# Kernel optimization log

Measured on AMD Instinct MI355X. Metric: run time of the kernel, lower is better.

The kernel has to match this reference:

```python
import math
import jax, jax.numpy as jnp
import numpy as np

B, T, D, H, L = 8, 2048, 1024, 16, 4
DK = D // H
EPS_LN = 1e-5
EPS_ATTN = 1e-6


def setup_inputs() -> dict:
    key = jax.random.key(0)
    ks = jax.random.split(key, 8)
    w = lambda k, shape: jax.random.normal(k, shape, dtype=jnp.float32) * 0.02
    return {
        'x_in': jax.random.normal(ks[0], (B, T, D), dtype=jnp.float32),
        'Wq': w(ks[1], (L, D, D)), 'bq': jnp.zeros((L, D), jnp.float32),
        'Wk': w(ks[2], (L, D, D)), 'bk': jnp.zeros((L, D), jnp.float32),
        'Wv': w(ks[3], (L, D, D)), 'bv': jnp.zeros((L, D), jnp.float32),
        'Wo': w(ks[4], (L, D, D)), 'bo': jnp.zeros((L, D), jnp.float32),
        'W1': w(ks[5], (L, D, 4 * D)), 'b1': jnp.zeros((L, 4 * D), jnp.float32),
        'W2': w(ks[6], (L, 4 * D, D)), 'b2': jnp.zeros((L, D), jnp.float32),
        'ln1_s': jnp.ones((L, D), jnp.float32), 'ln1_b': jnp.zeros((L, D), jnp.float32),
        'ln2_s': jnp.ones((L, D), jnp.float32), 'ln2_b': jnp.zeros((L, D), jnp.float32),
        'lnf_s': jnp.ones((D,), jnp.float32), 'lnf_b': jnp.zeros((D,), jnp.float32),
    }


def _layernorm(x, scale, bias):
    mu = jnp.mean(x, axis=-1, keepdims=True)
    var = jnp.mean(jnp.square(x - mu), axis=-1, keepdims=True)
    return (x - mu) * jax.lax.rsqrt(var + EPS_LN) * scale + bias


def _sinusoidal_pos_emb(t, d):
    # fairseq/MulT-style: sin half then cos half, positions start at 1 (padding_idx+1)
    half = d // 2
    freq = jnp.exp(jnp.arange(half, dtype=jnp.float32) * (-math.log(10000.0) / (half - 1)))
    pos = (jnp.arange(t, dtype=jnp.float32) + 1.0)[:, None] * freq[None, :]  # (T, half)
    return jnp.concatenate([jnp.sin(pos), jnp.cos(pos)], axis=-1)  # (T, D)


def _linear_attention(q, k, v):
    # q,k,v: (B, T, H, DK). elu+1 feature map, non-causal linear attention.
    qp = jax.nn.elu(q) + 1.0
    kp = jax.nn.elu(k) + 1.0
    kv = jnp.einsum('bshd,bshm->bhmd', kp, v)          # (B, H, DK_v, DK)
    ksum = jnp.sum(kp, axis=1)                          # (B, H, DK)
    z = 1.0 / (jnp.einsum('blhd,bhd->blh', qp, ksum) + EPS_ATTN)
    return jnp.einsum('blhd,bhmd,blh->blhm', qp, kv, z)  # (B, T, H, DK)


def _encoder_layer(x, Wq, bq, Wk, bk, Wv, bv, Wo, bo, W1, b1, W2, b2, ln1_s, ln1_b, ln2_s, ln2_b):
    b, t, d = x.shape
    # pre-LN self-attention block
    h = _layernorm(x, ln1_s, ln1_b)
    q = (h @ Wq + bq).reshape(b, t, H, DK)
    k = (h @ Wk + bk).reshape(b, t, H, DK)
    v = (h @ Wv + bv).reshape(b, t, H, DK)
    attn = _linear_attention(q, k, v).reshape(b, t, d)
    x = x + (attn @ Wo + bo)
    # pre-LN FFN block
    h = _layernorm(x, ln2_s, ln2_b)
    h = jax.nn.relu(h @ W1 + b1) @ W2 + b2
    return x + h


def reference(x_in, Wq, bq, Wk, bk, Wv, bv, Wo, bo, W1, b1, W2, b2,
              ln1_s, ln1_b, ln2_s, ln2_b, lnf_s, lnf_b):
    b, t, d = x_in.shape
    x = math.sqrt(d) * x_in + _sinusoidal_pos_emb(t, d)[None, :, :]
    for i in range(L):
        x = _encoder_layer(x, Wq[i], bq[i], Wk[i], bk[i], Wv[i], bv[i], Wo[i], bo[i],
                           W1[i], b1[i], W2[i], b2[i], ln1_s[i], ln1_b[i], ln2_s[i], ln2_b[i])
    return _layernorm(x, lnf_s, lnf_b)
```

## Files before the change

### kernel.cpp

```cpp
#include <hip/hip_runtime.h>
#include <cstdint>

#define BSZ   8
#define TSEQ  2048
#define DMOD  1024
#define NROWS 16384
#define NHEAD 16
#define DHEAD 64

__device__ __forceinline__ float bf2f(unsigned short h) {
  union { unsigned int u; float f; } a; a.u = ((unsigned int)h) << 16; return a.f;
}
__device__ __forceinline__ unsigned short f2bf(float f) {
  union { float f; unsigned int u; } a; a.f = f;
  unsigned int u = a.u;
  u += 0x7fffu + ((u >> 16) & 1u);
  return (unsigned short)(u >> 16);
}

typedef __bf16 bf16x8 __attribute__((ext_vector_type(8)));
typedef float  f32x4  __attribute__((ext_vector_type(4)));

typedef const __attribute__((address_space(1))) void* gas_ptr;
typedef __attribute__((address_space(3))) void*       las_ptr;

__device__ __forceinline__ void gl_lds16(const void* g, void* l) {
  __builtin_amdgcn_global_load_lds((gas_ptr)g, (las_ptr)l, 16, 0, 0);
}

__global__ __launch_bounds__(256) void transpose_cvt(const float* __restrict__ src,
                                                     unsigned short* __restrict__ dst,
                                                     int K, int N) {
  __shared__ float tile[32][33];
  const int n0 = blockIdx.x * 32, k0 = blockIdx.y * 32;
  const int tx = threadIdx.x, ty = threadIdx.y;
#pragma unroll
  for (int r = 0; r < 4; ++r)
    tile[ty + r * 8][tx] = src[(size_t)(k0 + ty + r * 8) * N + n0 + tx];
  __syncthreads();
#pragma unroll
  for (int r = 0; r < 4; ++r)
    dst[(size_t)(n0 + ty + r * 8) * K + k0 + tx] = f2bf(tile[tx][ty + r * 8]);
}

__global__ __launch_bounds__(256) void concat_bias(const float* __restrict__ bq,
                                                   const float* __restrict__ bk,
                                                   const float* __restrict__ bv,
                                                   float* __restrict__ out) {
  int i = blockIdx.x * 256 + threadIdx.x;
  int l = i / 3072, c = i - l * 3072;
  float v;
  if (c < 1024)       v = bq[l * 1024 + c];
  else if (c < 2048)  v = bk[l * 1024 + c - 1024];
  else                v = bv[l * 1024 + c - 2048];
  out[i] = v;
}

__global__ __launch_bounds__(256) void embed_k(const float* __restrict__ xin,
                                               float* __restrict__ x) {
  const size_t row = blockIdx.x;
  const int t = blockIdx.x & (TSEQ - 1);
  const int tid = threadIdx.x;
  const int c = tid * 4;
  float4 xv = ((const float4*)(xin + row * DMOD))[tid];
  float o[4];
  float xs[4] = { xv.x, xv.y, xv.z, xv.w };
#pragma unroll
  for (int j = 0; j < 4; ++j) {
    int dd = c + j;
    int i = dd & 511;
    float fr = expf(-0.0180241494559221f * (float)i);
    float ang = (float)(t + 1) * fr;
    float pe = (dd < 512) ? sinf(ang) : cosf(ang);
    o[j] = 32.0f * xs[j] + pe;
  }
  float4 ov = { o[0], o[1], o[2], o[3] };
  ((float4*)(x + row * DMOD))[tid] = ov;
}

__global__ __launch_bounds__(256) void ln_k(const float* __restrict__ x,
                                            const float* __restrict__ gam,
                                            const float* __restrict__ bet,
                                            unsigned short* __restrict__ outH) {
  const int row = blockIdx.x;
  const int tid = threadIdx.x;
  const float4 xv = ((const float4*)(x + (size_t)row * DMOD))[tid];
  float sum = xv.x + xv.y + xv.z + xv.w;
  float sq  = xv.x * xv.x + xv.y * xv.y + xv.z * xv.z + xv.w * xv.w;
#pragma unroll
  for (int o = 32; o; o >>= 1) { sum += __shfl_xor(sum, o); sq += __shfl_xor(sq, o); }
  __shared__ float s1[4], s2[4];
  const int wid = tid >> 6, lane = tid & 63;
  if (lane == 0) { s1[wid] = sum; s2[wid] = sq; }
  __syncthreads();
  sum = s1[0] + s1[1] + s1[2] + s1[3];
  sq  = s2[0] + s2[1] + s2[2] + s2[3];
  const float mu = sum * (1.0f / 1024.0f);
  const float var = sq * (1.0f / 1024.0f) - mu * mu;
  const float rs = rsqrtf(var + 1e-5f);
  const float4 g = ((const float4*)gam)[tid];
  const float4 b = ((const float4*)bet)[tid];
  union { unsigned short s[4]; uint2 u; } p;
  p.s[0] = f2bf((xv.x - mu) * rs * g.x + b.x);
  p.s[1] = f2bf((xv.y - mu) * rs * g.y + b.y);
  p.s[2] = f2bf((xv.z - mu) * rs * g.z + b.z);
  p.s[3] = f2bf((xv.w - mu) * rs * g.w + b.w);
  ((uint2*)(outH + (size_t)row * DMOD))[tid] = p.u;
}

template <int FINAL>
__global__ __launch_bounds__(256) void addln_k(float* __restrict__ x,
                                               const unsigned short* y,
                                               const float* __restrict__ gam,
                                               const float* __restrict__ bet,
                                               unsigned short* outH, float* outF) {
  const int row = blockIdx.x;
  const int tid = threadIdx.x;
  float4 xv = ((const float4*)(x + (size_t)row * DMOD))[tid];
  union { uint2 u; unsigned short s[4]; } yv;
  yv.u = ((const uint2*)(y + (size_t)row * DMOD))[tid];
  xv.x += bf2f(yv.s[0]); xv.y += bf2f(yv.s[1]);
  xv.z += bf2f(yv.s[2]); xv.w += bf2f(yv.s[3]);
  float sum = xv.x + xv.y + xv.z + xv.w;
  float sq  = xv.x * xv.x + xv.y * xv.y + xv.z * xv.z + xv.w * xv.w;
#pragma unroll
  for (int o = 32; o; o >>= 1) { sum += __shfl_xor(sum, o); sq += __shfl_xor(sq, o); }
  __shared__ float s1[4], s2[4];
  const int wid = tid >> 6, lane = tid & 63;
  if (lane == 0) { s1[wid] = sum; s2[wid] = sq; }
  __syncthreads();
  sum = s1[0] + s1[1] + s1[2] + s1[3];
  sq  = s2[0] + s2[1] + s2[2] + s2[3];
  const float mu = sum * (1.0f / 1024.0f);
  const float var = sq * (1.0f / 1024.0f) - mu * mu;
  const float rs = rsqrtf(var + 1e-5f);
  const float4 g = ((const float4*)gam)[tid];
  const float4 b = ((const float4*)bet)[tid];
  float o0 = (xv.x - mu) * rs * g.x + b.x;
  float o1 = (xv.y - mu) * rs * g.y + b.y;
  float o2 = (xv.z - mu) * rs * g.z + b.z;
  float o3 = (xv.w - mu) * rs * g.w + b.w;
  if (FINAL) {
    float4 ov = { o0, o1, o2, o3 };
    ((float4*)(outF + (size_t)row * DMOD))[tid] = ov;
  } else {
    ((float4*)(x + (size_t)row * DMOD))[tid] = xv;
    union { unsigned short s[4]; uint2 u; } p;
    p.s[0] = f2bf(o0); p.s[1] = f2bf(o1); p.s[2] = f2bf(o2); p.s[3] = f2bf(o3);
    ((uint2*)(outH + (size_t)row * DMOD))[tid] = p.u;
  }
}

template <int RELU>
__global__ __launch_bounds__(512, 2) void gemm256(const unsigned short* __restrict__ A,
                                                  const unsigned short* __restrict__ Bt,
                                                  const float* __restrict__ bias,
                                                  unsigned short* __restrict__ outH,
                                                  int M, int N, int K, int lda) {
  __shared__ __align__(16) unsigned short sm[65536];
  const int tid = threadIdx.x;
  const int wid = tid >> 6, lane = tid & 63;
  const int wm = wid >> 2, wn = wid & 3;

  const int nwg = gridDim.x;
  const int q = nwg >> 3, r = nwg & 7;
  const int xcd = blockIdx.x & 7, sub = blockIdx.x >> 3;
  const int wg = (xcd < r ? xcd * (q + 1) : r * (q + 1) + (xcd - r) * q) + sub;
  const int nbm = M >> 8;
  const int bm = wg % nbm, bn = wg / nbm;
  const long m0 = (long)bm << 8, n0 = (long)bn << 8;

  const int srow = tid >> 3;
  const int cswz = (tid & 7) ^ (srow & 7);
  const unsigned short* Ag = A + (size_t)(m0 + srow) * lda + cswz * 8;
  const unsigned short* Bg = Bt + (size_t)(n0 + srow) * K + cswz * 8;
  char* const smb = (char*)sm;
  const int nT = K >> 6;

#define STAGE_A(t, h)                                                              \
  do {                                                                             \
    const unsigned short* g_ = Ag + (size_t)(t) * 64 + (size_t)((h) * 128) * lda;  \
    char* d_ = smb + (((t) & 1) << 15) + ((h) << 14) + (wid << 10);                \
    gl_lds16(g_, d_);                                                              \
    gl_lds16(g_ + ((size_t)lda << 6), d_ + 8192);                                  \
  } while (0)
#define STAGE_B(t, h)                                                              \
  do {                                                                             \
    const unsigned short* g_ = Bg + (size_t)(t) * 64 + (size_t)((h) * 128) * K;    \
    char* d_ = smb + 65536 + (((t) & 1) << 15) + ((h) << 14) + (wid << 10);        \
    gl_lds16(g_, d_);                                                              \
    gl_lds16(g_ + ((size_t)K << 6), d_ + 8192);                                    \
  } while (0)

  const int fr = lane & 15;
  const int aswz = ((lane >> 4) ^ (lane & 7)) << 4;
  const int aoff = (wm * 128 + fr) * 128;
  const int boff = (wn * 64 + fr) * 128;

  f32x4 acc[8][4] = {};
  bf16x8 a0[4][2], a1[4][2], bfr[4][2];

  STAGE_A(0, 0); STAGE_A(0, 1); STAGE_B(0, 0); STAGE_B(0, 1);
  if (nT > 1) {
    STAGE_B(1, 1); STAGE_B(1, 0); STAGE_A(1, 1);
    asm volatile("s_waitcnt vmcnt(6)" ::: "memory");
  } else {
    asm volatile("s_waitcnt vmcnt(0)" ::: "memory");
  }
  asm volatile("s_barrier" ::: "memory");

  for (int T = 0; T < nT; ++T) {
    const char* Ab = smb + ((T & 1) << 15);
    const char* Bb = Ab + 65536;

#pragma unroll
    for (int i = 0; i < 4; ++i)
#pragma unroll
      for (int ks = 0; ks < 2; ++ks) {
        a0[i][ks]  = *(const bf16x8*)(Ab + aoff + i * 2048 + (aswz ^ (ks << 6)));
        bfr[i][ks] = *(const bf16x8*)(Bb + boff + i * 2048 + (aswz ^ (ks << 6)));
      }
    if (T + 1 < nT) STAGE_A(T + 1, 0);
    asm volatile("s_barrier" ::: "memory");
    asm volatile("s_waitcnt lgkmcnt(0)" ::: "memory");
    __builtin_amdgcn_sched_barrier(0);
    __builtin_amdgcn_s_setprio(1);
#pragma unroll
    for (int i = 0; i < 4; ++i)
#pragma unroll
      for (int j = 0; j < 2; ++j)
#pragma unroll
        for (int ks = 0; ks < 2; ++ks)
          acc[i][j] = __builtin_amdgcn_mfma_f32_16x16x32_bf16(a0[i][ks], bfr[j][ks], acc[i][j], 0, 0, 0);
    __builtin_amdgcn_s_setprio(0);
    __builtin_amdgcn_sched_barrier(0);
    asm volatile("s_barrier" ::: "memory");

#pragma unroll
    for (int i = 0; i < 2; ++i)
#pragma unroll
      for (int ks = 0; ks < 2; ++ks)
        a1[i][ks] = *(const bf16x8*)(Ab + aoff + (i + 4) * 2048 + (aswz ^ (ks << 6)));
    if (T + 2 < nT) STAGE_B(T + 2, 1);
    asm volatile("s_barrier" ::: "memory");
    __builtin_amdgcn_sched_barrier(0);
    __builtin_amdgcn_s_setprio(1);
#pragma unroll
    for (int i = 0; i < 4; ++i)
#pragma unroll
      for (int j = 2; j < 4; ++j)
#pragma unroll
        for (int ks = 0; ks < 2; ++ks)
          acc[i][j] = __builtin_amdgcn_mfma_f32_16x16x32_bf16(a0[i][ks], bfr[j][ks], acc[i][j], 0, 0, 0);
    __builtin_amdgcn_s_setprio(0);
    __builtin_amdgcn_sched_barrier(0);
    asm volatile("s_barrier" ::: "memory");

#pragma unroll
    for (int i = 2; i < 4; ++i)
#pragma unroll
      for (int ks = 0; ks < 2; ++ks)
        a1[i][ks] = *(const bf16x8*)(Ab + aoff + (i + 4) * 2048 + (aswz ^ (ks << 6)));
    if (T + 2 < nT) STAGE_B(T + 2, 0);
    asm volatile("s_barrier" ::: "memory");
    asm volatile("s_waitcnt lgkmcnt(0)" ::: "memory");
    __builtin_amdgcn_sched_barrier(0);
    __builtin_amdgcn_s_setprio(1);
#pragma unroll
    for (int i = 0; i < 4; ++i)
#pragma unroll
      for (int j = 0; j < 2; ++j)
#pragma unroll
        for (int ks = 0; ks < 2; ++ks)
          acc[i + 4][j] = __builtin_amdgcn_mfma_f32_16x16x32_bf16(a1[i][ks], bfr[j][ks], acc[i + 4][j], 0, 0, 0);
    __builtin_amdgcn_s_setprio(0);
    __builtin_amdgcn_sched_barrier(0);
    asm volatile("s_barrier" ::: "memory");

    if (T + 2 < nT) {
      STAGE_A(T + 2, 1);
      asm volatile("s_waitcnt vmcnt(6)" ::: "memory");
    } else {
      asm volatile("s_waitcnt vmcnt(0)" ::: "memory");
    }
    asm volatile("s_barrier" ::: "memory");
    __builtin_amdgcn_sched_barrier(0);
    __builtin_amdgcn_s_setprio(1);
#pragma unroll
    for (int i = 0; i < 4; ++i)
#pragma unroll
      for (int j = 2; j < 4; ++j)
#pragma unroll
        for (int ks = 0; ks < 2; ++ks)
          acc[i + 4][j] = __builtin_amdgcn_mfma_f32_16x16x32_bf16(a1[i][ks], bfr[j][ks], acc[i + 4][j], 0, 0, 0);
    __builtin_amdgcn_s_setprio(0);
    __builtin_amdgcn_sched_barrier(0);
    asm volatile("s_barrier" ::: "memory");
  }
#undef STAGE_A
#undef STAGE_B

  asm volatile("s_waitcnt vmcnt(0)" ::: "memory");
  __syncthreads();
  {
    const int cq = lane >> 4, cn = lane & 15;
#pragma unroll
    for (int j = 0; j < 4; ++j) {
      const float bb = bias[n0 + wn * 64 + j * 16 + cn];
#pragma unroll
      for (int i = 0; i < 8; ++i)
#pragma unroll
        for (int v = 0; v < 4; ++v) {
          const int row = wm * 128 + i * 16 + cq * 4 + v;
          const int col = wn * 64 + j * 16 + cn;
          float val = acc[i][j][v] + bb;
          if (RELU) val = fmaxf(val, 0.0f);
          sm[row * 256 + (col ^ ((row & 12) << 2))] = f2bf(val);
        }
    }
  }
  __syncthreads();
#pragma unroll
  for (int it = 0; it < 16; ++it) {
    const int row = it * 16 + (tid >> 5);
    const int ch = tid & 31;
    const int chs = ch ^ ((row & 12) >> 1);
    const uint4 val = *(const uint4*)(sm + row * 256 + chs * 8);
    *(uint4*)(outH + (size_t)(m0 + row) * N + n0 + ch * 8) = val;
  }
}

__global__ __launch_bounds__(256) void attn_kv_partial(const unsigned short* __restrict__ qkv,
                                                       float* __restrict__ kvp,
                                                       float* __restrict__ ksump) {
  const int bh = blockIdx.x, tc = blockIdx.y;
  const int b = bh >> 4, h = bh & 15;
  const int tid = threadIdx.x;
  const int m = tid & 63, wid = tid >> 6;
  __shared__ float ks[32][64];
  __shared__ float vs[32][64];
  float acc[16];
#pragma unroll
  for (int j = 0; j < 16; ++j) acc[j] = 0.0f;
  float ksacc = 0.0f;
  const int tt = tid >> 3;
  const int dsb = (tid & 7) * 8;
  const size_t base = ((size_t)b * TSEQ + tc * 256) * 3072;
  const int kcol = 1024 + h * 64 + dsb, vcol = 2048 + h * 64 + dsb;
  for (int sc = 0; sc < 8; ++sc) {
    __syncthreads();
    const size_t roff = base + (size_t)(sc * 32 + tt) * 3072;
    uint4 kb = *(const uint4*)(qkv + roff + kcol);
    uint4 vb = *(const uint4*)(qkv + roff + vcol);
    const unsigned int* kw = (const unsigned int*)&kb;
    const unsigned int* vw = (const unsigned int*)&vb;
#pragma unroll
    for (int w2 = 0; w2 < 4; ++w2) {
      float k0 = bf2f((unsigned short)(kw[w2] & 0xffffu));
      float k1 = bf2f((unsigned short)(kw[w2] >> 16));
      ks[tt][dsb + 2 * w2]     = (k0 > 0.f) ? k0 + 1.f : expf(k0);
      ks[tt][dsb + 2 * w2 + 1] = (k1 > 0.f) ? k1 + 1.f : expf(k1);
      vs[tt][dsb + 2 * w2]     = bf2f((unsigned short)(vw[w2] & 0xffffu));
      vs[tt][dsb + 2 * w2 + 1] = bf2f((unsigned short)(vw[w2] >> 16));
    }
    __syncthreads();
#pragma unroll 4
    for (int t2 = 0; t2 < 32; ++t2) {
      float vv = vs[t2][m];
#pragma unroll
      for (int j = 0; j < 16; ++j) acc[j] += ks[t2][wid * 16 + j] * vv;
      if (tid < 64) ksacc += ks[t2][tid];
    }
  }
  float* dst = kvp + (size_t)(tc * 128 + bh) * 4096;
#pragma unroll
  for (int j = 0; j < 16; ++j) dst[(wid * 16 + j) * 64 + m] = acc[j];
  if (tid < 64) ksump[(size_t)(tc * 128 + bh) * 64 + tid] = ksacc;
}

__global__ __launch_bounds__(256) void attn_kv_reduce(const float* __restrict__ kvp,
                                                      const float* __restrict__ ksump,
                                                      float* __restrict__ kvf,
                                                      float* __restrict__ ksumf) {
  const int bh = blockIdx.x;
  const int tid = threadIdx.x;
  for (int i = tid; i < 4096; i += 256) {
    float s = 0.f;
#pragma unroll
    for (int tc = 0; tc < 8; ++tc) s += kvp[(size_t)(tc * 128 + bh) * 4096 + i];
    kvf[(size_t)bh * 4096 + i] = s;
  }
  if (tid < 64) {
    float s = 0.f;
#pragma unroll
    for (int tc = 0; tc < 8; ++tc) s += ksump[(size_t)(tc * 128 + bh) * 64 + tid];
    ksumf[bh * 64 + tid] = s;
  }
}

__global__ __launch_bounds__(256) void attn_out_k(const unsigned short* __restrict__ qkv,
                                                  const float* __restrict__ kvf,
                                                  const float* __restrict__ ksumf,
                                                  unsigned short* __restrict__ qkvO) {
  const int bh = blockIdx.x, tcb = blockIdx.y;
  const int b = bh >> 4, h = bh & 15;
  const int tid = threadIdx.x, wid = tid >> 6, lane = tid & 63;
  __shared__ float kvs[4096];
  __shared__ float kss[64];
  __shared__ float qps[4][64];
  for (int i = tid; i < 1024; i += 256)
    ((float4*)kvs)[i] = ((const float4*)(kvf + (size_t)bh * 4096))[i];
  if (tid < 64) kss[tid] = ksumf[bh * 64 + tid];
  __syncthreads();
  for (int it = 0; it < 64; ++it) {
    const int t = tcb * 256 + wid * 64 + it;
    const size_t row = (size_t)b * TSEQ + t;
    float q = bf2f(qkv[row * 3072 + h * 64 + lane]);
    float qp = (q > 0.f) ? q + 1.f : expf(q);
    float r = qp * kss[lane];
#pragma unroll
    for (int o = 32; o; o >>= 1) r += __shfl_xor(r, o);
    const float z = 1.0f / (r + 1e-6f);
    qps[wid][lane] = qp;
    float o = 0.f;
#pragma unroll
    for (int d = 0; d < 64; ++d) o += qps[wid][d] * kvs[d * 64 + lane];
    qkvO[row * 3072 + h * 64 + lane] = f2bf(o * z);
  }
}

extern "C" void kernel_launch(void* const* d_in, const int* in_sizes, int n_in,
                              void* d_out, int out_size, void* d_ws, size_t ws_size,
                              hipStream_t stream) {
  const float* x_in = (const float*)d_in[0];
  const float* Wq = (const float*)d_in[1];
  const float* bq = (const float*)d_in[2];
  const float* Wk = (const float*)d_in[3];
  const float* bk = (const float*)d_in[4];
  const float* Wv = (const float*)d_in[5];
  const float* bv = (const float*)d_in[6];
  const float* Wo = (const float*)d_in[7];
  const float* bo = (const float*)d_in[8];
  const float* W1 = (const float*)d_in[9];
  const float* b1 = (const float*)d_in[10];
  const float* W2 = (const float*)d_in[11];
  const float* b2 = (const float*)d_in[12];
  const float* ln1s = (const float*)d_in[13];
  const float* ln1b = (const float*)d_in[14];
  const float* ln2s = (const float*)d_in[15];
  const float* ln2b = (const float*)d_in[16];
  const float* lnfs = (const float*)d_in[17];
  const float* lnfb = (const float*)d_in[18];

  float* x = (float*)d_out;

  char* w = (char*)d_ws;
  unsigned short* hh    = (unsigned short*)(w + 0);
  unsigned short* qkv   = (unsigned short*)(w + 33554432);
  unsigned short* h1    = (unsigned short*)(w + 33554432);
  unsigned short* qkvwt = (unsigned short*)(w + 167772160);
  unsigned short* wot   = (unsigned short*)(w + 174063616);
  unsigned short* w1t   = (unsigned short*)(w + 176160768);
  unsigned short* w2t   = (unsigned short*)(w + 184549376);
  float*          bqkv  = (float*)(w + 192937984);
  float*          kvp   = (float*)(w + 192987136);
  float*          ksump = (float*)(w + 209764352);
  float*          kvf   = (float*)(w + 210026496);
  float*          ksumf = (float*)(w + 212123648);
  (void)ws_size; (void)in_sizes; (void)n_in; (void)out_size;

  dim3 b256(256);
  dim3 b512(512);
  dim3 tb(32, 8);
  concat_bias<<<48, b256, 0, stream>>>(bq, bk, bv, bqkv);
  embed_k<<<NROWS, b256, 0, stream>>>(x_in, x);
  ln_k<<<NROWS, b256, 0, stream>>>(x, ln1s, ln1b, hh);

  for (int l = 0; l < 4; ++l) {
    transpose_cvt<<<dim3(32, 32), tb, 0, stream>>>(Wq + (size_t)l * 1048576, qkvwt,           1024, 1024);
    transpose_cvt<<<dim3(32, 32), tb, 0, stream>>>(Wk + (size_t)l * 1048576, qkvwt + 1048576, 1024, 1024);
    transpose_cvt<<<dim3(32, 32), tb, 0, stream>>>(Wv + (size_t)l * 1048576, qkvwt + 2097152, 1024, 1024);
    transpose_cvt<<<dim3(32, 32), tb, 0, stream>>>(Wo + (size_t)l * 1048576, wot, 1024, 1024);
    transpose_cvt<<<dim3(128, 32), tb, 0, stream>>>(W1 + (size_t)l * 4194304, w1t, 1024, 4096);
    transpose_cvt<<<dim3(32, 128), tb, 0, stream>>>(W2 + (size_t)l * 4194304, w2t, 4096, 1024);

    gemm256<0><<<dim3(64 * 12), b512, 0, stream>>>(hh, qkvwt, bqkv + l * 3072, qkv,
                                                   NROWS, 3072, 1024, 1024);
    attn_kv_partial<<<dim3(128, 8), b256, 0, stream>>>(qkv, kvp, ksump);
    attn_kv_reduce<<<128, b256, 0, stream>>>(kvp, ksump, kvf, ksumf);
    attn_out_k<<<dim3(128, 8), b256, 0, stream>>>(qkv, kvf, ksumf, qkv);
    gemm256<0><<<dim3(64 * 4), b512, 0, stream>>>(qkv, wot, bo + l * 1024, hh,
                                                  NROWS, 1024, 1024, 3072);
    addln_k<0><<<NROWS, b256, 0, stream>>>(x, hh, ln2s + l * 1024, ln2b + l * 1024, hh, nullptr);
    gemm256<1><<<dim3(64 * 16), b512, 0, stream>>>(hh, w1t, b1 + l * 4096, h1,
                                                   NROWS, 4096, 1024, 1024);
    gemm256<0><<<dim3(64 * 4), b512, 0, stream>>>(h1, w2t, b2 + l * 1024, hh,
                                                  NROWS, 1024, 4096, 4096);
    if (l < 3)
      addln_k<0><<<NROWS, b256, 0, stream>>>(x, hh, ln1s + (l + 1) * 1024, ln1b + (l + 1) * 1024,
                                             hh, nullptr);
    else
      addln_k<1><<<NROWS, b256, 0, stream>>>(x, hh, lnfs, lnfb, nullptr, x);
  }
}
```

Measured before the change: 2.833 ms.

## Restructure GEMM main loop to prefetch next-tile LDS fragments, batch attn_out rows

```diff
diff --git a/kernel.cpp b/kernel.cpp
--- a/kernel.cpp
+++ b/kernel.cpp
@@ -27,6 +27,10 @@
 __device__ __forceinline__ void gl_lds16(const void* g, void* l) {
   __builtin_amdgcn_global_load_lds((gas_ptr)g, (las_ptr)l, 16, 0, 0);
 }
+
+#define BAR()        asm volatile("s_barrier" ::: "memory")
+#define WAIT_LGKM(n) asm volatile("s_waitcnt lgkmcnt(" #n ")" ::: "memory")
+#define WAIT_VM(n)   asm volatile("s_waitcnt vmcnt(" #n ")" ::: "memory")
 
 __global__ __launch_bounds__(256) void transpose_cvt(const float* __restrict__ src,
                                                      unsigned short* __restrict__ dst,
@@ -198,72 +202,61 @@
   const int boff = (wn * 64 + fr) * 128;
 
   f32x4 acc[8][4] = {};
-  bf16x8 a0[4][2], a1[4][2], bfr[4][2];
+  bf16x8 a0[4][2], a1[4][2], b01[2][2], b23[2][2];
 
   STAGE_A(0, 0); STAGE_A(0, 1); STAGE_B(0, 0); STAGE_B(0, 1);
   if (nT > 1) {
-    STAGE_B(1, 1); STAGE_B(1, 0); STAGE_A(1, 1);
-    asm volatile("s_waitcnt vmcnt(6)" ::: "memory");
+    STAGE_B(1, 0); STAGE_B(1, 1); STAGE_A(1, 0); STAGE_A(1, 1);
+    WAIT_VM(8);
   } else {
-    asm volatile("s_waitcnt vmcnt(0)" ::: "memory");
-  }
-  asm volatile("s_barrier" ::: "memory");
+    WAIT_VM(0);
+  }
+  BAR();
+#pragma unroll
+  for (int i = 0; i < 4; ++i)
+#pragma unroll
+    for (int ks = 0; ks < 2; ++ks)
+      a0[i][ks] = *(const bf16x8*)(smb + aoff + i * 2048 + (aswz ^ (ks << 6)));
+#pragma unroll
+  for (int j = 0; j < 2; ++j)
+#pragma unroll
+    for (int ks = 0; ks < 2; ++ks)
+      b01[j][ks] = *(const bf16x8*)(smb + 65536 + boff + j * 2048 + (aswz ^ (ks << 6)));
 
   for (int T = 0; T < nT; ++T) {
-    const char* Ab = smb + ((T & 1) << 15);
-    const char* Bb = Ab + 65536;
-
+    const char* Ab  = smb + ((T & 1) << 15);
+    const char* Bb  = Ab + 65536;
+    const char* Ab2 = smb + (((T + 1) & 1) << 15);
+    const char* Bb2 = Ab2 + 65536;
+
+#pragma unroll
+    for (int j = 0; j < 2; ++j)
+#pragma unroll
+      for (int ks = 0; ks < 2; ++ks)
+        b23[j][ks] = *(const bf16x8*)(Bb + boff + (j + 2) * 2048 + (aswz ^ (ks << 6)));
+    BAR();
+    WAIT_LGKM(4);
+    __builtin_amdgcn_sched_barrier(0);
+    __builtin_amdgcn_s_setprio(1);
 #pragma unroll
     for (int i = 0; i < 4; ++i)
 #pragma unroll
-      for (int ks = 0; ks < 2; ++ks) {
-        a0[i][ks]  = *(const bf16x8*)(Ab + aoff + i * 2048 + (aswz ^ (ks << 6)));
-        bfr[i][ks] = *(const bf16x8*)(Bb + boff + i * 2048 + (aswz ^ (ks << 6)));
-      }
-    if (T + 1 < nT) STAGE_A(T + 1, 0);
-    asm volatile("s_barrier" ::: "memory");
-    asm volatile("s_waitcnt lgkmcnt(0)" ::: "memory");
-    __builtin_amdgcn_sched_barrier(0);
-    __builtin_amdgcn_s_setprio(1);
+      for (int j = 0; j < 2; ++j)
+#pragma unroll
+        for (int ks = 0; ks < 2; ++ks)
+          acc[i][j] = __builtin_amdgcn_mfma_f32_16x16x32_bf16(a0[i][ks], b01[j][ks], acc[i][j], 0, 0, 0);
+    __builtin_amdgcn_s_setprio(0);
+    __builtin_amdgcn_sched_barrier(0);
+    BAR();
+
 #pragma unroll
     for (int i = 0; i < 4; ++i)
-#pragma unroll
-      for (int j = 0; j < 2; ++j)
-#pragma unroll
-        for (int ks = 0; ks < 2; ++ks)
-          acc[i][j] = __builtin_amdgcn_mfma_f32_16x16x32_bf16(a0[i][ks], bfr[j][ks], acc[i][j], 0, 0, 0);
-    __builtin_amdgcn_s_setprio(0);
-    __builtin_amdgcn_sched_barrier(0);
-    asm volatile("s_barrier" ::: "memory");
-
-#pragma unroll
-    for (int i = 0; i < 2; ++i)
-#pragma unroll
-      for (int ks = 0; ks < 2; ++ks)
-        a1[i][ks] = *(const bf16x8*)(Ab + aoff + (i + 4) * 2048 + (aswz ^ (ks << 6)));
-    if (T + 2 < nT) STAGE_B(T + 2, 1);
-    asm volatile("s_barrier" ::: "memory");
-    __builtin_amdgcn_sched_barrier(0);
-    __builtin_amdgcn_s_setprio(1);
-#pragma unroll
-    for (int i = 0; i < 4; ++i)
-#pragma unroll
-      for (int j = 2; j < 4; ++j)
-#pragma unroll
-        for (int ks = 0; ks < 2; ++ks)
-          acc[i][j] = __builtin_amdgcn_mfma_f32_16x16x32_bf16(a0[i][ks], bfr[j][ks], acc[i][j], 0, 0, 0);
-    __builtin_amdgcn_s_setprio(0);
-    __builtin_amdgcn_sched_barrier(0);
-    asm volatile("s_barrier" ::: "memory");
-
-#pragma unroll
-    for (int i = 2; i < 4; ++i)
 #pragma unroll
       for (int ks = 0; ks < 2; ++ks)
         a1[i][ks] = *(const bf16x8*)(Ab + aoff + (i + 4) * 2048 + (aswz ^ (ks << 6)));
     if (T + 2 < nT) STAGE_B(T + 2, 0);
-    asm volatile("s_barrier" ::: "memory");
-    asm volatile("s_waitcnt lgkmcnt(0)" ::: "memory");
+    BAR();
+    WAIT_LGKM(8);
     __builtin_amdgcn_sched_barrier(0);
     __builtin_amdgcn_s_setprio(1);
 #pragma unroll
@@ -272,35 +265,68 @@
       for (int j = 0; j < 2; ++j)
 #pragma unroll
         for (int ks = 0; ks < 2; ++ks)
-          acc[i + 4][j] = __builtin_amdgcn_mfma_f32_16x16x32_bf16(a1[i][ks], bfr[j][ks], acc[i + 4][j], 0, 0, 0);
+          acc[i][j + 2] = __builtin_amdgcn_mfma_f32_16x16x32_bf16(a0[i][ks], b23[j][ks], acc[i][j + 2], 0, 0, 0);
     __builtin_amdgcn_s_setprio(0);
     __builtin_amdgcn_sched_barrier(0);
-    asm volatile("s_barrier" ::: "memory");
-
+    BAR();
+
+    WAIT_LGKM(0);
     if (T + 2 < nT) {
-      STAGE_A(T + 2, 1);
-      asm volatile("s_waitcnt vmcnt(6)" ::: "memory");
+      STAGE_B(T + 2, 1); STAGE_A(T + 2, 0);
+      WAIT_VM(6);
+    } else if (T + 1 < nT) {
+      WAIT_VM(0);
+    }
+    BAR();
+    if (T + 1 < nT) {
+#pragma unroll
+      for (int i = 0; i < 4; ++i)
+#pragma unroll
+        for (int ks = 0; ks < 2; ++ks)
+          a0[i][ks] = *(const bf16x8*)(Ab2 + aoff + i * 2048 + (aswz ^ (ks << 6)));
+      WAIT_LGKM(8);
     } else {
-      asm volatile("s_waitcnt vmcnt(0)" ::: "memory");
-    }
-    asm volatile("s_barrier" ::: "memory");
+      WAIT_LGKM(0);
+    }
     __builtin_amdgcn_sched_barrier(0);
     __builtin_amdgcn_s_setprio(1);
 #pragma unroll
     for (int i = 0; i < 4; ++i)
 #pragma unroll
-      for (int j = 2; j < 4; ++j)
+      for (int j = 0; j < 2; ++j)
 #pragma unroll
         for (int ks = 0; ks < 2; ++ks)
-          acc[i + 4][j] = __builtin_amdgcn_mfma_f32_16x16x32_bf16(a1[i][ks], bfr[j][ks], acc[i + 4][j], 0, 0, 0);
+          acc[i + 4][j] = __builtin_amdgcn_mfma_f32_16x16x32_bf16(a1[i][ks], b01[j][ks], acc[i + 4][j], 0, 0, 0);
     __builtin_amdgcn_s_setprio(0);
     __builtin_amdgcn_sched_barrier(0);
-    asm volatile("s_barrier" ::: "memory");
+    BAR();
+
+    if (T + 1 < nT) {
+#pragma unroll
+      for (int j = 0; j < 2; ++j)
+#pragma unroll
+        for (int ks = 0; ks < 2; ++ks)
+          b01[j][ks] = *(const bf16x8*)(Bb2 + boff + j * 2048 + (aswz ^ (ks << 6)));
+    }
+    if (T + 2 < nT) STAGE_A(T + 2, 1);
+    BAR();
+    __builtin_amdgcn_sched_barrier(0);
+    __builtin_amdgcn_s_setprio(1);
+#pragma unroll
+    for (int i = 0; i < 4; ++i)
+#pragma unroll
+      for (int j = 0; j < 2; ++j)
+#pragma unroll
+        for (int ks = 0; ks < 2; ++ks)
+          acc[i + 4][j + 2] = __builtin_amdgcn_mfma_f32_16x16x32_bf16(a1[i][ks], b23[j][ks], acc[i + 4][j + 2], 0, 0, 0);
+    __builtin_amdgcn_s_setprio(0);
+    __builtin_amdgcn_sched_barrier(0);
+    BAR();
   }
 #undef STAGE_A
 #undef STAGE_B
 
-  asm volatile("s_waitcnt vmcnt(0)" ::: "memory");
+  WAIT_VM(0);
   __syncthreads();
   {
     const int cq = lane >> 4, cn = lane & 15;
@@ -407,25 +433,39 @@
   const int tid = threadIdx.x, wid = tid >> 6, lane = tid & 63;
   __shared__ float kvs[4096];
   __shared__ float kss[64];
-  __shared__ float qps[4][64];
+  __shared__ float qps[4][4][64];
   for (int i = tid; i < 1024; i += 256)
     ((float4*)kvs)[i] = ((const float4*)(kvf + (size_t)bh * 4096))[i];
   if (tid < 64) kss[tid] = ksumf[bh * 64 + tid];
   __syncthreads();
-  for (int it = 0; it < 64; ++it) {
-    const int t = tcb * 256 + wid * 64 + it;
-    const size_t row = (size_t)b * TSEQ + t;
-    float q = bf2f(qkv[row * 3072 + h * 64 + lane]);
-    float qp = (q > 0.f) ? q + 1.f : expf(q);
-    float r = qp * kss[lane];
-#pragma unroll
-    for (int o = 32; o; o >>= 1) r += __shfl_xor(r, o);
-    const float z = 1.0f / (r + 1e-6f);
-    qps[wid][lane] = qp;
-    float o = 0.f;
-#pragma unroll
-    for (int d = 0; d < 64; ++d) o += qps[wid][d] * kvs[d * 64 + lane];
-    qkvO[row * 3072 + h * 64 + lane] = f2bf(o * z);
+  for (int it = 0; it < 64; it += 4) {
+    float zr[4];
+#pragma unroll
+    for (int r = 0; r < 4; ++r) {
+      const int t = tcb * 256 + wid * 64 + it + r;
+      const size_t row = (size_t)b * TSEQ + t;
+      float qv = bf2f(qkv[row * 3072 + h * 64 + lane]);
+      float qp = (qv > 0.f) ? qv + 1.f : expf(qv);
+      float rs = qp * kss[lane];
+#pragma unroll
+      for (int o = 32; o; o >>= 1) rs += __shfl_xor(rs, o);
+      zr[r] = 1.0f / (rs + 1e-6f);
+      qps[wid][r][lane] = qp;
+    }
+    float o0 = 0.f, o1 = 0.f, o2 = 0.f, o3 = 0.f;
+#pragma unroll 8
+    for (int d = 0; d < 64; ++d) {
+      const float kvv = kvs[d * 64 + lane];
+      o0 += qps[wid][0][d] * kvv;
+      o1 += qps[wid][1][d] * kvv;
+      o2 += qps[wid][2][d] * kvv;
+      o3 += qps[wid][3][d] * kvv;
+    }
+    const size_t row0 = (size_t)b * TSEQ + tcb * 256 + wid * 64 + it;
+    qkvO[(row0 + 0) * 3072 + h * 64 + lane] = f2bf(o0 * zr[0]);
+    qkvO[(row0 + 1) * 3072 + h * 64 + lane] = f2bf(o1 * zr[1]);
+    qkvO[(row0 + 2) * 3072 + h * 64 + lane] = f2bf(o2 * zr[2]);
+    qkvO[(row0 + 3) * 3072 + h * 64 + lane] = f2bf(o3 * zr[3]);
   }
 }
 
```

New measurement: 2.833 ms. No clear change (-0.0%).
